# Kernel optimization log

Hardware: AMD Instinct MI355X
Metric: run time of the kernel (lower is better)

Reference implementation:

```python
import jax, jax.numpy as jnp
import numpy as np

H, D = 12, 768
DH = D // H  # 64

def setup_inputs() -> dict:
    key = jax.random.key(0)
    ks = jax.random.split(key, 9)
    s = 0.02
    x  = jax.random.normal(ks[0], (8, 1024, D), dtype=jnp.float32)
    Wq = jax.random.normal(ks[1], (H, D, DH), dtype=jnp.float32) * s
    Wk = jax.random.normal(ks[2], (H, D, DH), dtype=jnp.float32) * s
    Wv = jax.random.normal(ks[3], (H, D, DH), dtype=jnp.float32) * s
    bq = jax.random.normal(ks[4], (H, DH), dtype=jnp.float32) * s
    bk = jax.random.normal(ks[5], (H, DH), dtype=jnp.float32) * s
    bv = jax.random.normal(ks[6], (H, DH), dtype=jnp.float32) * s
    Wo = jax.random.normal(ks[7], (D, D), dtype=jnp.float32) * s
    bo = jax.random.normal(ks[8], (D,), dtype=jnp.float32) * s
    return {"x": x, "Wq": Wq, "Wk": Wk, "Wv": Wv, "bq": bq, "bk": bk, "bv": bv, "Wo": Wo, "bo": bo}

def reference(x, Wq, Wk, Wv, bq, bk, bv, Wo, bo):
    # x: [B,S,D]; per-head projections batched over heads: [B,H,S,DH]
    q = jnp.einsum('bsd,hde->bhse', x, Wq) + bq[None, :, None, :]
    k = jnp.einsum('bsd,hde->bhse', x, Wk) + bk[None, :, None, :]
    v = jnp.einsum('bsd,hde->bhse', x, Wv) + bv[None, :, None, :]
    scores = jnp.einsum('bhse,bhte->bhst', q, k) / jnp.sqrt(jnp.float32(DH))
    probs = jax.nn.softmax(scores, axis=-1)  # dropout is identity (p=0 / eval)
    ctx = jnp.einsum('bhst,bhte->bhse', probs, v)  # [B,H,S,DH]
    B, _, S, _ = ctx.shape
    # concat heads along feature dim (head order matches torch cat order)
    ctx = jnp.transpose(ctx, (0, 2, 1, 3)).reshape(B, S, H * DH)
    out = jnp.einsum('bsd,de->bse', ctx, Wo) + bo
    return out
```

## Files before the change

### kernel.cpp

```cpp
#include <hip/hip_runtime.h>
#include <math.h>


constexpr int NB  = 8;
constexpr int SEQ = 1024;
constexpr int NH  = 12;
constexpr int DM  = 768;
constexpr int DHD = 64;
constexpr int MROWS = NB * SEQ;
constexpr int NQKV  = 3 * NH * DHD;

typedef __attribute__((ext_vector_type(8))) short short8;
typedef __attribute__((ext_vector_type(4))) float f32x4;

#define MFMA16(a,b,c) __builtin_amdgcn_mfma_f32_16x16x32_bf16((a),(b),(c),0,0,0)

#if __has_builtin(__builtin_amdgcn_exp2f)
#define EXP2(x) __builtin_amdgcn_exp2f(x)
#else
#define EXP2(x) exp2f(x)
#endif

__device__ __forceinline__ unsigned short f2bf(float f) {
    unsigned u = __float_as_uint(f);
    return (unsigned short)((u + 0x7fffu + ((u >> 16) & 1u)) >> 16);
}
__device__ __forceinline__ unsigned short f2bf_fast(float f) {
    return (unsigned short)((__float_as_uint(f) + 0x8000u) >> 16);
}

__device__ __forceinline__ void gl_lds16(const unsigned short* g, unsigned short* l) {
    __builtin_amdgcn_global_load_lds(
        (const __attribute__((address_space(1))) void*)g,
        (__attribute__((address_space(3))) void*)l, 16, 0, 0);
}

__device__ __forceinline__ void stageK(unsigned short* lds, const unsigned short* gbase,
                                       int i, int ln, int ldg) {
    int r    = i * 8 + (ln >> 3);
    int cpos = ln & 7;
    int cdat = (cpos - r) & 7;
    gl_lds16(gbase + (size_t)r * ldg + cdat * 8, lds + i * 512);
}
__device__ __forceinline__ short8 ldK(const unsigned short* buf, int row, int chunk) {
    int c = (chunk + row) & 7;
    return *(const short8*)&buf[row * 64 + c * 8];
}

__global__ __launch_bounds__(256) void prep_k(
    const float* __restrict__ x,
    const float* __restrict__ Wq, const float* __restrict__ Wk,
    const float* __restrict__ Wv, const float* __restrict__ Wo,
    unsigned short* __restrict__ xb, unsigned short* __restrict__ wt,
    unsigned short* __restrict__ wot) {
    __shared__ float tb[64][65];
    const int blk = blockIdx.x, tid = threadIdx.x;
    if (blk < 6144) {
        const int i = blk * 256 + tid;
        float4 v = ((const float4*)x)[i];
        ushort4 o;
        o.x = f2bf(v.x); o.y = f2bf(v.y); o.z = f2bf(v.z); o.w = f2bf(v.w);
        ((ushort4*)xb)[i] = o;
        return;
    }
    const int t = blk - 6144;
    const int job = t / 144, lb = t % 144;
    const float* W;
    unsigned short* dst;
    int C, r0, c0;
    if (job < 3) {
        const float* Ws = (job == 0) ? Wq : (job == 1 ? Wk : Wv);
        const int h = lb / 12, rb = lb % 12;
        W = Ws + (size_t)h * (DM * DHD);
        dst = wt + (size_t)(job * 12 + h) * (DM * DHD);
        C = DHD; r0 = rb * 64; c0 = 0;
    } else {
        W = Wo; dst = wot; C = DM;
        r0 = (lb / 12) * 64; c0 = (lb % 12) * 64;
    }
    const int rr = tid >> 2, cc = (tid & 3) * 16;
#pragma unroll
    for (int j = 0; j < 16; j += 4) {
        float4 v = *(const float4*)&W[(size_t)(r0 + rr) * C + c0 + cc + j];
        tb[rr][cc + j + 0] = v.x;
        tb[rr][cc + j + 1] = v.y;
        tb[rr][cc + j + 2] = v.z;
        tb[rr][cc + j + 3] = v.w;
    }
    __syncthreads();
#pragma unroll
    for (int j = 0; j < 16; ++j)
        dst[(size_t)(c0 + rr) * DM + r0 + cc + j] = f2bf(tb[cc + j][rr]);
}

__global__ __launch_bounds__(256, 3) void qkv_mfma_k(
    const unsigned short* __restrict__ xb, const unsigned short* __restrict__ wt,
    const float* __restrict__ bq, const float* __restrict__ bk, const float* __restrict__ bv,
    unsigned short* __restrict__ qb, unsigned short* __restrict__ kb,
    unsigned short* __restrict__ vT) {
    __shared__ unsigned short Ah[128 * 64], Bh[128 * 64];

    const int tid = threadIdx.x;
    const int wv = tid >> 6, ln = tid & 63, quad = ln >> 4, lnid = ln & 15;
    const int wvm = wv >> 1, wvn = wv & 1;
    const int row0 = blockIdx.x * 128, col0 = blockIdx.y * 128;
    const int sel = (col0 >= 2 * DM) ? 2 : (col0 >= DM ? 1 : 0);

    f32x4 acc[4][4];
#pragma unroll
    for (int i = 0; i < 4; ++i)
#pragma unroll
        for (int j = 0; j < 4; ++j) acc[i][j] = (f32x4){0.f, 0.f, 0.f, 0.f};

    const unsigned short* Ahg = xb + (size_t)row0 * DM;
    const unsigned short* Bhg = wt + (size_t)col0 * DM;
    constexpr int NIT = DM / 64;

    if (sel < 2) {
        for (int it = 0; it < NIT; ++it) {
            const int kc = it * 64;
            __syncthreads();
#pragma unroll
            for (int c = 0; c < 4; ++c) {
                stageK(Ah, Ahg + kc, wv * 4 + c, ln, DM);
                stageK(Bh, Bhg + kc, wv * 4 + c, ln, DM);
            }
            __syncthreads();
#pragma unroll
            for (int ks = 0; ks < 2; ++ks) {
                short8 a[4], b[4];
#pragma unroll
                for (int i = 0; i < 4; ++i)
                    a[i] = ldK(Ah, wvm * 64 + i * 16 + lnid, ks * 4 + quad);
#pragma unroll
                for (int j = 0; j < 4; ++j)
                    b[j] = ldK(Bh, wvn * 64 + j * 16 + lnid, ks * 4 + quad);
#pragma unroll
                for (int j = 0; j < 4; ++j)
#pragma unroll
                    for (int i = 0; i < 4; ++i)
                        acc[j][i] = MFMA16(b[j], a[i], acc[j][i]);
            }
        }
        const float scale = (sel == 0) ? 0.18033688011112042f : 1.0f;
        const float* bias = (sel == 0) ? bq : bk;
        unsigned short* oh = (sel == 0) ? qb : kb;
#pragma unroll
        for (int et = 0; et < 4; ++et) {
            const int e = col0 + wvn * 64 + et * 16 + quad * 4;
            const int he = e - sel * DM;
            const int hh2 = he >> 6, ee = he & 63;
            float4 bs = *(const float4*)&bias[he];
#pragma unroll
            for (int st = 0; st < 4; ++st) {
                const int srow = row0 + wvm * 64 + st * 16 + lnid;
                const int bb = srow >> 10, ss = srow & (SEQ - 1);
                ushort4 pk;
                pk.x = f2bf((acc[et][st][0] + bs.x) * scale);
                pk.y = f2bf((acc[et][st][1] + bs.y) * scale);
                pk.z = f2bf((acc[et][st][2] + bs.z) * scale);
                pk.w = f2bf((acc[et][st][3] + bs.w) * scale);
                *(ushort4*)&oh[((size_t)(bb * NH + hh2) * SEQ + ss) * DHD + ee] = pk;
            }
        }
    } else {
        for (int it = 0; it < NIT; ++it) {
            const int kc = it * 64;
            __syncthreads();
#pragma unroll
            for (int c = 0; c < 4; ++c) {
                stageK(Ah, Ahg + kc, wv * 4 + c, ln, DM);
                stageK(Bh, Bhg + kc, wv * 4 + c, ln, DM);
            }
            __syncthreads();
#pragma unroll
            for (int ks = 0; ks < 2; ++ks) {
                short8 a[4], b[4];
#pragma unroll
                for (int i = 0; i < 4; ++i)
                    a[i] = ldK(Ah, wvm * 64 + i * 16 + lnid, ks * 4 + quad);
#pragma unroll
                for (int j = 0; j < 4; ++j)
                    b[j] = ldK(Bh, wvn * 64 + j * 16 + lnid, ks * 4 + quad);
#pragma unroll
                for (int i = 0; i < 4; ++i)
#pragma unroll
                    for (int j = 0; j < 4; ++j)
                        acc[i][j] = MFMA16(a[i], b[j], acc[i][j]);
            }
        }
#pragma unroll
        for (int i = 0; i < 4; ++i) {
#pragma unroll
            for (int j = 0; j < 4; ++j) {
                const int col = col0 + wvn * 64 + j * 16 + lnid;
                const int he = col - 2 * DM;
                const int hh2 = he >> 6, ee = he & 63;
                const float bs = bv[he];
                const int srow = row0 + wvm * 64 + i * 16 + quad * 4;
                const int bb = srow >> 10, ss = srow & (SEQ - 1);
                ushort4 pk;
                pk.x = f2bf(acc[i][j][0] + bs);
                pk.y = f2bf(acc[i][j][1] + bs);
                pk.z = f2bf(acc[i][j][2] + bs);
                pk.w = f2bf(acc[i][j][3] + bs);
                *(ushort4*)&vT[((size_t)(bb * NH + hh2) * DHD + ee) * SEQ + ss] = pk;
            }
        }
    }
}

__global__ __launch_bounds__(512, 6) void attn_mfma_k(
    const unsigned short* __restrict__ qb, const unsigned short* __restrict__ kb,
    const unsigned short* __restrict__ vT, unsigned short* __restrict__ ctb) {
    __shared__ unsigned short ksh[2][64 * 64], vsm[2][64 * 64];
    __shared__ unsigned short ps[128 * 64];

    const int tid = threadIdx.x;
    const int wv = tid >> 6, ln = tid & 63, quad = ln >> 4, lnid = ln & 15;
    const int bhid = blockIdx.x % 96, qt = blockIdx.x / 96;
    const int b = bhid / NH, h = bhid % NH;
    const int q0 = qt * 128;
    const unsigned short* qhb = qb + (size_t)bhid * (SEQ * DHD);
    const unsigned short* khb = kb + (size_t)bhid * (SEQ * DHD);
    const unsigned short* vTb = vT + (size_t)bhid * (DHD * SEQ);

    const int prow = wv * 16 + lnid;

    short8 qf[2];
#pragma unroll
    for (int ks_ = 0; ks_ < 2; ++ks_)
        qf[ks_] = *(const short8*)(qhb + (size_t)(q0 + prow) * DHD + ks_ * 32 + quad * 8);

    f32x4 ctx[4];
#pragma unroll
    for (int j = 0; j < 4; ++j) ctx[j] = (f32x4){0.f, 0.f, 0.f, 0.f};
    float lsum = 0.f;

    stageK(ksh[0], khb, wv, ln, DHD);
    stageK(vsm[0], vTb, wv, ln, SEQ);

    for (int kt = 0; kt < SEQ / 64; ++kt) {
        const int cur = kt & 1;
        __syncthreads();
        if (kt + 1 < SEQ / 64) {
            stageK(ksh[cur ^ 1], khb + (kt + 1) * 64 * DHD, wv, ln, DHD);
            stageK(vsm[cur ^ 1], vTb + (kt + 1) * 64, wv, ln, SEQ);
        }

        f32x4 sc[4];
#pragma unroll
        for (int j = 0; j < 4; ++j) sc[j] = (f32x4){0.f, 0.f, 0.f, 0.f};
#pragma unroll
        for (int ks_ = 0; ks_ < 2; ++ks_) {
#pragma unroll
            for (int nt = 0; nt < 4; ++nt) {
                short8 kf = ldK(ksh[cur], nt * 16 + lnid, ks_ * 4 + quad);
                sc[nt] = MFMA16(kf, qf[ks_], sc[nt]);
            }
        }

#pragma unroll
        for (int nt = 0; nt < 4; ++nt) {
            float p0 = EXP2(sc[nt][0]);
            float p1 = EXP2(sc[nt][1]);
            float p2 = EXP2(sc[nt][2]);
            float p3 = EXP2(sc[nt][3]);
            lsum += (p0 + p1) + (p2 + p3);
            ushort4 pw;
            pw.x = f2bf_fast(p0);
            pw.y = f2bf_fast(p1);
            pw.z = f2bf_fast(p2);
            pw.w = f2bf_fast(p3);
            const int cpos = (2 * nt + (quad >> 1) + prow) & 7;
            *(ushort4*)&ps[prow * 64 + cpos * 8 + (quad & 1) * 4] = pw;
        }

#pragma unroll
        for (int kvs = 0; kvs < 2; ++kvs) {
            short8 pf = ldK(ps, prow, kvs * 4 + quad);
#pragma unroll
            for (int dt = 0; dt < 4; ++dt) {
                short8 vf = ldK(vsm[cur], dt * 16 + lnid, kvs * 4 + quad);
                ctx[dt] = MFMA16(vf, pf, ctx[dt]);
            }
        }
    }

    float s = lsum;
    s += __shfl_xor(s, 16, 64);
    s += __shfl_xor(s, 32, 64);
    const float inv = 1.0f / s;
    const int srow = b * SEQ + q0 + prow;
#pragma unroll
    for (int dt = 0; dt < 4; ++dt) {
        ushort4 pk;
        pk.x = f2bf(ctx[dt][0] * inv);
        pk.y = f2bf(ctx[dt][1] * inv);
        pk.z = f2bf(ctx[dt][2] * inv);
        pk.w = f2bf(ctx[dt][3] * inv);
        *(ushort4*)&ctb[(size_t)srow * DM + h * DHD + dt * 16 + quad * 4] = pk;
    }
}

__global__ __launch_bounds__(256, 3) void out_mfma_k(
    const unsigned short* __restrict__ ctb, const unsigned short* __restrict__ wot,
    const float* __restrict__ bo, float* __restrict__ out) {
    __shared__ unsigned short Ah[128 * 64], Bh[64 * 64];

    const int tid = threadIdx.x;
    const int wv = tid >> 6, ln = tid & 63, quad = ln >> 4, lnid = ln & 15;
    const int wvm = wv >> 1, wvn = wv & 1;
    const int row0 = blockIdx.x * 128, col0 = blockIdx.y * 64;

    f32x4 acc[2][4];
#pragma unroll
    for (int j = 0; j < 2; ++j)
#pragma unroll
        for (int i = 0; i < 4; ++i) acc[j][i] = (f32x4){0.f, 0.f, 0.f, 0.f};

    const unsigned short* Ahg = ctb + (size_t)row0 * DM;
    const unsigned short* Bhg = wot + (size_t)col0 * DM;

    constexpr int NIT = DM / 64;
    for (int it = 0; it < NIT; ++it) {
        const int kc = it * 64;
        __syncthreads();
#pragma unroll
        for (int c = 0; c < 4; ++c) stageK(Ah, Ahg + kc, wv * 4 + c, ln, DM);
#pragma unroll
        for (int c = 0; c < 2; ++c) stageK(Bh, Bhg + kc, wv * 2 + c, ln, DM);
        __syncthreads();
#pragma unroll
        for (int ks = 0; ks < 2; ++ks) {
            short8 a[4], b[2];
#pragma unroll
            for (int i = 0; i < 4; ++i)
                a[i] = ldK(Ah, wvm * 64 + i * 16 + lnid, ks * 4 + quad);
#pragma unroll
            for (int j = 0; j < 2; ++j)
                b[j] = ldK(Bh, wvn * 32 + j * 16 + lnid, ks * 4 + quad);
#pragma unroll
            for (int j = 0; j < 2; ++j)
#pragma unroll
                for (int i = 0; i < 4; ++i)
                    acc[j][i] = MFMA16(b[j], a[i], acc[j][i]);
        }
    }

#pragma unroll
    for (int jt = 0; jt < 2; ++jt) {
        const int colb = col0 + wvn * 32 + jt * 16 + quad * 4;
        float4 bs = *(const float4*)&bo[colb];
#pragma unroll
        for (int it = 0; it < 4; ++it) {
            const int srow = row0 + wvm * 64 + it * 16 + lnid;
            float4 o;
            o.x = acc[jt][it][0] + bs.x;
            o.y = acc[jt][it][1] + bs.y;
            o.z = acc[jt][it][2] + bs.z;
            o.w = acc[jt][it][3] + bs.w;
            *(float4*)&out[(size_t)srow * DM + colb] = o;
        }
    }
}

extern "C" void kernel_launch(void* const* d_in, const int* in_sizes, int n_in,
                              void* d_out, int out_size, void* d_ws, size_t ws_size,
                              hipStream_t stream) {
    const float* x  = (const float*)d_in[0];
    const float* Wq = (const float*)d_in[1];
    const float* Wk = (const float*)d_in[2];
    const float* Wv = (const float*)d_in[3];
    const float* bq = (const float*)d_in[4];
    const float* bk = (const float*)d_in[5];
    const float* bv = (const float*)d_in[6];
    const float* Wo = (const float*)d_in[7];
    const float* bo = (const float*)d_in[8];
    float* out = (float*)d_out;

    char* w = (char*)d_ws;
    const size_t elsX = (size_t)MROWS * DM;
    const size_t elsQ = (size_t)NB * NH * SEQ * DHD;
    unsigned short* xb  = (unsigned short*)w;
    unsigned short* ctb = xb;
    size_t off = elsX * 2;
    unsigned short* wt  = (unsigned short*)(w + off); off += (size_t)NQKV * DM * 2;
    unsigned short* wot = (unsigned short*)(w + off); off += (size_t)DM * DM * 2;
    unsigned short* qbp = (unsigned short*)(w + off); off += elsQ * 2;
    unsigned short* kbp = (unsigned short*)(w + off); off += elsQ * 2;
    unsigned short* vTp = (unsigned short*)(w + off); off += elsQ * 2;

    prep_k<<<dim3(6144 + 576), 256, 0, stream>>>(x, Wq, Wk, Wv, Wo, xb, wt, wot);
    qkv_mfma_k<<<dim3(MROWS / 128, NQKV / 128), 256, 0, stream>>>(
        xb, wt, bq, bk, bv, qbp, kbp, vTp);
    attn_mfma_k<<<dim3(768), 512, 0, stream>>>(qbp, kbp, vTp, ctb);
    out_mfma_k<<<dim3(MROWS / 128, DM / 64), 256, 0, stream>>>(ctb, wot, bo, out);
}
```

Before: 192.1 us.

## Give each attention wave two 16-row query groups to reuse K/V fragments

The attention kernel moves from 8 waves of 16 query rows to 4 waves of 32 query rows. Each wave keeps two sets of Q fragments and accumulators, so every K and V fragment loaded from LDS feeds two MFMAs. This cuts LDS reads per MFMA and the number of waves in each block, and each wave now does twice the staging work. The cost is higher register pressure and less wave-level parallelism for hiding latency, with launch bounds changed to (256, 3).

```diff
diff --git a/kernel.cpp b/kernel.cpp
--- a/kernel.cpp
+++ b/kernel.cpp
@@ -210,7 +210,7 @@
     }
 }
 
-__global__ __launch_bounds__(512, 6) void attn_mfma_k(
+__global__ __launch_bounds__(256, 3) void attn_mfma_k(
     const unsigned short* __restrict__ qb, const unsigned short* __restrict__ kb,
     const unsigned short* __restrict__ vT, unsigned short* __restrict__ ctb) {
     __shared__ unsigned short ksh[2][64 * 64], vsm[2][64 * 64];
@@ -225,81 +225,103 @@
     const unsigned short* khb = kb + (size_t)bhid * (SEQ * DHD);
     const unsigned short* vTb = vT + (size_t)bhid * (DHD * SEQ);
 
-    const int prow = wv * 16 + lnid;
-
-    short8 qf[2];
-#pragma unroll
-    for (int ks_ = 0; ks_ < 2; ++ks_)
-        qf[ks_] = *(const short8*)(qhb + (size_t)(q0 + prow) * DHD + ks_ * 32 + quad * 8);
-
-    f32x4 ctx[4];
-#pragma unroll
-    for (int j = 0; j < 4; ++j) ctx[j] = (f32x4){0.f, 0.f, 0.f, 0.f};
-    float lsum = 0.f;
-
-    stageK(ksh[0], khb, wv, ln, DHD);
-    stageK(vsm[0], vTb, wv, ln, SEQ);
+    const int prow0 = wv * 32 + lnid;
+
+    short8 qf[2][2];
+#pragma unroll
+    for (int rg = 0; rg < 2; ++rg)
+#pragma unroll
+        for (int ks_ = 0; ks_ < 2; ++ks_)
+            qf[rg][ks_] = *(const short8*)(qhb +
+                (size_t)(q0 + prow0 + rg * 16) * DHD + ks_ * 32 + quad * 8);
+
+    f32x4 ctx[2][4];
+#pragma unroll
+    for (int rg = 0; rg < 2; ++rg)
+#pragma unroll
+        for (int j = 0; j < 4; ++j) ctx[rg][j] = (f32x4){0.f, 0.f, 0.f, 0.f};
+    float lsum0 = 0.f, lsum1 = 0.f;
+
+    stageK(ksh[0], khb, wv * 2 + 0, ln, DHD);
+    stageK(ksh[0], khb, wv * 2 + 1, ln, DHD);
+    stageK(vsm[0], vTb, wv * 2 + 0, ln, SEQ);
+    stageK(vsm[0], vTb, wv * 2 + 1, ln, SEQ);
 
     for (int kt = 0; kt < SEQ / 64; ++kt) {
         const int cur = kt & 1;
         __syncthreads();
         if (kt + 1 < SEQ / 64) {
-            stageK(ksh[cur ^ 1], khb + (kt + 1) * 64 * DHD, wv, ln, DHD);
-            stageK(vsm[cur ^ 1], vTb + (kt + 1) * 64, wv, ln, SEQ);
-        }
-
-        f32x4 sc[4];
-#pragma unroll
-        for (int j = 0; j < 4; ++j) sc[j] = (f32x4){0.f, 0.f, 0.f, 0.f};
+            stageK(ksh[cur ^ 1], khb + (kt + 1) * 64 * DHD, wv * 2 + 0, ln, DHD);
+            stageK(ksh[cur ^ 1], khb + (kt + 1) * 64 * DHD, wv * 2 + 1, ln, DHD);
+            stageK(vsm[cur ^ 1], vTb + (kt + 1) * 64, wv * 2 + 0, ln, SEQ);
+            stageK(vsm[cur ^ 1], vTb + (kt + 1) * 64, wv * 2 + 1, ln, SEQ);
+        }
+
+        f32x4 sc[2][4];
+#pragma unroll
+        for (int rg = 0; rg < 2; ++rg)
+#pragma unroll
+            for (int j = 0; j < 4; ++j) sc[rg][j] = (f32x4){0.f, 0.f, 0.f, 0.f};
 #pragma unroll
         for (int ks_ = 0; ks_ < 2; ++ks_) {
 #pragma unroll
             for (int nt = 0; nt < 4; ++nt) {
                 short8 kf = ldK(ksh[cur], nt * 16 + lnid, ks_ * 4 + quad);
-                sc[nt] = MFMA16(kf, qf[ks_], sc[nt]);
-            }
-        }
-
-#pragma unroll
-        for (int nt = 0; nt < 4; ++nt) {
-            float p0 = EXP2(sc[nt][0]);
-            float p1 = EXP2(sc[nt][1]);
-            float p2 = EXP2(sc[nt][2]);
-            float p3 = EXP2(sc[nt][3]);
-            lsum += (p0 + p1) + (p2 + p3);
-            ushort4 pw;
-            pw.x = f2bf_fast(p0);
-            pw.y = f2bf_fast(p1);
-            pw.z = f2bf_fast(p2);
-            pw.w = f2bf_fast(p3);
-            const int cpos = (2 * nt + (quad >> 1) + prow) & 7;
-            *(ushort4*)&ps[prow * 64 + cpos * 8 + (quad & 1) * 4] = pw;
+                sc[0][nt] = MFMA16(kf, qf[0][ks_], sc[0][nt]);
+                sc[1][nt] = MFMA16(kf, qf[1][ks_], sc[1][nt]);
+            }
+        }
+
+#pragma unroll
+        for (int rg = 0; rg < 2; ++rg) {
+            const int prow = prow0 + rg * 16;
+#pragma unroll
+            for (int nt = 0; nt < 4; ++nt) {
+                float p0 = EXP2(sc[rg][nt][0]);
+                float p1 = EXP2(sc[rg][nt][1]);
+                float p2 = EXP2(sc[rg][nt][2]);
+                float p3 = EXP2(sc[rg][nt][3]);
+                if (rg == 0) lsum0 += (p0 + p1) + (p2 + p3);
+                else         lsum1 += (p0 + p1) + (p2 + p3);
+                ushort4 pw;
+                pw.x = f2bf_fast(p0);
+                pw.y = f2bf_fast(p1);
+                pw.z = f2bf_fast(p2);
+                pw.w = f2bf_fast(p3);
+                const int cpos = (2 * nt + (quad >> 1) + prow) & 7;
+                *(ushort4*)&ps[prow * 64 + cpos * 8 + (quad & 1) * 4] = pw;
+            }
         }
 
 #pragma unroll
         for (int kvs = 0; kvs < 2; ++kvs) {
-            short8 pf = ldK(ps, prow, kvs * 4 + quad);
+            short8 pf0 = ldK(ps, prow0,      kvs * 4 + quad);
+            short8 pf1 = ldK(ps, prow0 + 16, kvs * 4 + quad);
 #pragma unroll
             for (int dt = 0; dt < 4; ++dt) {
                 short8 vf = ldK(vsm[cur], dt * 16 + lnid, kvs * 4 + quad);
-                ctx[dt] = MFMA16(vf, pf, ctx[dt]);
-            }
-        }
-    }
-
-    float s = lsum;
-    s += __shfl_xor(s, 16, 64);
-    s += __shfl_xor(s, 32, 64);
-    const float inv = 1.0f / s;
-    const int srow = b * SEQ + q0 + prow;
-#pragma unroll
-    for (int dt = 0; dt < 4; ++dt) {
-        ushort4 pk;
-        pk.x = f2bf(ctx[dt][0] * inv);
-        pk.y = f2bf(ctx[dt][1] * inv);
-        pk.z = f2bf(ctx[dt][2] * inv);
-        pk.w = f2bf(ctx[dt][3] * inv);
-        *(ushort4*)&ctb[(size_t)srow * DM + h * DHD + dt * 16 + quad * 4] = pk;
+                ctx[0][dt] = MFMA16(vf, pf0, ctx[0][dt]);
+                ctx[1][dt] = MFMA16(vf, pf1, ctx[1][dt]);
+            }
+        }
+    }
+
+#pragma unroll
+    for (int rg = 0; rg < 2; ++rg) {
+        float s = (rg == 0) ? lsum0 : lsum1;
+        s += __shfl_xor(s, 16, 64);
+        s += __shfl_xor(s, 32, 64);
+        const float inv = 1.0f / s;
+        const int srow = b * SEQ + q0 + prow0 + rg * 16;
+#pragma unroll
+        for (int dt = 0; dt < 4; ++dt) {
+            ushort4 pk;
+            pk.x = f2bf(ctx[rg][dt][0] * inv);
+            pk.y = f2bf(ctx[rg][dt][1] * inv);
+            pk.z = f2bf(ctx[rg][dt][2] * inv);
+            pk.w = f2bf(ctx[rg][dt][3] * inv);
+            *(ushort4*)&ctb[(size_t)srow * DM + h * DHD + dt * 16 + quad * 4] = pk;
+        }
     }
 }
 
@@ -394,6 +416,6 @@
     prep_k<<<dim3(6144 + 576), 256, 0, stream>>>(x, Wq, Wk, Wv, Wo, xb, wt, wot);
     qkv_mfma_k<<<dim3(MROWS / 128, NQKV / 128), 256, 0, stream>>>(
         xb, wt, bq, bk, bv, qbp, kbp, vTp);
-    attn_mfma_k<<<dim3(768), 512, 0, stream>>>(qbp, kbp, vTp, ctb);
+    attn_mfma_k<<<dim3(768), 256, 0, stream>>>(qbp, kbp, vTp, ctb);
     out_mfma_k<<<dim3(MROWS / 128, DM / 64), 256, 0, stream>>>(ctb, wot, bo, out);
 }
```

After: 191.7 us. About the same (-0.2%).

## Switch attention to 32x32x16 MFMA with 256-query tiles per block

Applied to the files above, without the earlier changes.

The attention kernel now uses 32x32x16 bf16 MFMA instructions instead of 16x16x32, and each wave owns 32 query rows, so a block covers 256 queries and the grid is halved. Each K/V tile staged into LDS is therefore reused across twice as many queries, cutting global and LDS traffic per unit of work. In exchange the P buffer in LDS doubles, register pressure rises (16-wide accumulators), occupancy is lowered to 4 blocks, and only 384 blocks are launched, which may underfill the GPU.

```diff
diff --git a/kernel.cpp b/kernel.cpp
--- a/kernel.cpp
+++ b/kernel.cpp
@@ -12,8 +12,10 @@
 
 typedef __attribute__((ext_vector_type(8))) short short8;
 typedef __attribute__((ext_vector_type(4))) float f32x4;
+typedef __attribute__((ext_vector_type(16))) float f32x16;
 
 #define MFMA16(a,b,c) __builtin_amdgcn_mfma_f32_16x16x32_bf16((a),(b),(c),0,0,0)
+#define MFMA32(a,b,c) __builtin_amdgcn_mfma_f32_32x32x16_bf16((a),(b),(c),0,0,0)
 
 #if __has_builtin(__builtin_amdgcn_exp2f)
 #define EXP2(x) __builtin_amdgcn_exp2f(x)
@@ -210,31 +212,33 @@
     }
 }
 
-__global__ __launch_bounds__(512, 6) void attn_mfma_k(
+__global__ __launch_bounds__(512, 4) void attn_mfma_k(
     const unsigned short* __restrict__ qb, const unsigned short* __restrict__ kb,
     const unsigned short* __restrict__ vT, unsigned short* __restrict__ ctb) {
     __shared__ unsigned short ksh[2][64 * 64], vsm[2][64 * 64];
-    __shared__ unsigned short ps[128 * 64];
+    __shared__ unsigned short ps[256 * 64];
 
     const int tid = threadIdx.x;
-    const int wv = tid >> 6, ln = tid & 63, quad = ln >> 4, lnid = ln & 15;
+    const int wv = tid >> 6, ln = tid & 63, lo5 = ln & 31, hi = ln >> 5;
     const int bhid = blockIdx.x % 96, qt = blockIdx.x / 96;
     const int b = bhid / NH, h = bhid % NH;
-    const int q0 = qt * 128;
+    const int q0 = qt * 256;
     const unsigned short* qhb = qb + (size_t)bhid * (SEQ * DHD);
     const unsigned short* khb = kb + (size_t)bhid * (SEQ * DHD);
     const unsigned short* vTb = vT + (size_t)bhid * (DHD * SEQ);
 
-    const int prow = wv * 16 + lnid;
-
-    short8 qf[2];
-#pragma unroll
-    for (int ks_ = 0; ks_ < 2; ++ks_)
-        qf[ks_] = *(const short8*)(qhb + (size_t)(q0 + prow) * DHD + ks_ * 32 + quad * 8);
-
-    f32x4 ctx[4];
-#pragma unroll
-    for (int j = 0; j < 4; ++j) ctx[j] = (f32x4){0.f, 0.f, 0.f, 0.f};
+    const int wq = wv * 32 + lo5;
+
+    short8 qf[4];
+#pragma unroll
+    for (int ds = 0; ds < 4; ++ds)
+        qf[ds] = *(const short8*)(qhb + (size_t)(q0 + wq) * DHD + ds * 16 + hi * 8);
+
+    f32x16 ctx[2];
+#pragma unroll
+    for (int dt = 0; dt < 2; ++dt)
+#pragma unroll
+        for (int r = 0; r < 16; ++r) ctx[dt][r] = 0.f;
     float lsum = 0.f;
 
     stageK(ksh[0], khb, wv, ln, DHD);
@@ -248,58 +252,63 @@
             stageK(vsm[cur ^ 1], vTb + (kt + 1) * 64, wv, ln, SEQ);
         }
 
-        f32x4 sc[4];
-#pragma unroll
-        for (int j = 0; j < 4; ++j) sc[j] = (f32x4){0.f, 0.f, 0.f, 0.f};
-#pragma unroll
-        for (int ks_ = 0; ks_ < 2; ++ks_) {
-#pragma unroll
-            for (int nt = 0; nt < 4; ++nt) {
-                short8 kf = ldK(ksh[cur], nt * 16 + lnid, ks_ * 4 + quad);
-                sc[nt] = MFMA16(kf, qf[ks_], sc[nt]);
-            }
-        }
-
-#pragma unroll
-        for (int nt = 0; nt < 4; ++nt) {
-            float p0 = EXP2(sc[nt][0]);
-            float p1 = EXP2(sc[nt][1]);
-            float p2 = EXP2(sc[nt][2]);
-            float p3 = EXP2(sc[nt][3]);
-            lsum += (p0 + p1) + (p2 + p3);
-            ushort4 pw;
-            pw.x = f2bf_fast(p0);
-            pw.y = f2bf_fast(p1);
-            pw.z = f2bf_fast(p2);
-            pw.w = f2bf_fast(p3);
-            const int cpos = (2 * nt + (quad >> 1) + prow) & 7;
-            *(ushort4*)&ps[prow * 64 + cpos * 8 + (quad & 1) * 4] = pw;
-        }
-
-#pragma unroll
-        for (int kvs = 0; kvs < 2; ++kvs) {
-            short8 pf = ldK(ps, prow, kvs * 4 + quad);
-#pragma unroll
-            for (int dt = 0; dt < 4; ++dt) {
-                short8 vf = ldK(vsm[cur], dt * 16 + lnid, kvs * 4 + quad);
-                ctx[dt] = MFMA16(vf, pf, ctx[dt]);
-            }
-        }
-    }
-
-    float s = lsum;
-    s += __shfl_xor(s, 16, 64);
-    s += __shfl_xor(s, 32, 64);
+        f32x16 sc[2];
+#pragma unroll
+        for (int kk = 0; kk < 2; ++kk) {
+#pragma unroll
+            for (int r = 0; r < 16; ++r) sc[kk][r] = 0.f;
+#pragma unroll
+            for (int ds = 0; ds < 4; ++ds) {
+                short8 kf = ldK(ksh[cur], kk * 32 + lo5, ds * 2 + hi);
+                sc[kk] = MFMA32(kf, qf[ds], sc[kk]);
+            }
+        }
+
+#pragma unroll
+        for (int kk = 0; kk < 2; ++kk) {
+#pragma unroll
+            for (int m = 0; m < 4; ++m) {
+                float p0 = EXP2(sc[kk][4 * m + 0]);
+                float p1 = EXP2(sc[kk][4 * m + 1]);
+                float p2 = EXP2(sc[kk][4 * m + 2]);
+                float p3 = EXP2(sc[kk][4 * m + 3]);
+                lsum += (p0 + p1) + (p2 + p3);
+                ushort4 pw;
+                pw.x = f2bf_fast(p0);
+                pw.y = f2bf_fast(p1);
+                pw.z = f2bf_fast(p2);
+                pw.w = f2bf_fast(p3);
+                const int c = kk * 4 + m;
+                const int pc = (c + wq) & 7;
+                *(ushort4*)&ps[wq * 64 + pc * 8 + hi * 4] = pw;
+            }
+        }
+
+#pragma unroll
+        for (int step = 0; step < 4; ++step) {
+            short8 pf = ldK(ps, wq, step * 2 + hi);
+#pragma unroll
+            for (int dt = 0; dt < 2; ++dt) {
+                short8 vf = ldK(vsm[cur], dt * 32 + lo5, step * 2 + hi);
+                ctx[dt] = MFMA32(vf, pf, ctx[dt]);
+            }
+        }
+    }
+
+    float s = lsum + __shfl_xor(lsum, 32, 64);
     const float inv = 1.0f / s;
-    const int srow = b * SEQ + q0 + prow;
-#pragma unroll
-    for (int dt = 0; dt < 4; ++dt) {
-        ushort4 pk;
-        pk.x = f2bf(ctx[dt][0] * inv);
-        pk.y = f2bf(ctx[dt][1] * inv);
-        pk.z = f2bf(ctx[dt][2] * inv);
-        pk.w = f2bf(ctx[dt][3] * inv);
-        *(ushort4*)&ctb[(size_t)srow * DM + h * DHD + dt * 16 + quad * 4] = pk;
+    const int srow = b * SEQ + q0 + wq;
+#pragma unroll
+    for (int dt = 0; dt < 2; ++dt) {
+#pragma unroll
+        for (int m = 0; m < 4; ++m) {
+            ushort4 pk;
+            pk.x = f2bf(ctx[dt][4 * m + 0] * inv);
+            pk.y = f2bf(ctx[dt][4 * m + 1] * inv);
+            pk.z = f2bf(ctx[dt][4 * m + 2] * inv);
+            pk.w = f2bf(ctx[dt][4 * m + 3] * inv);
+            *(ushort4*)&ctb[(size_t)srow * DM + h * DHD + dt * 32 + m * 8 + hi * 4] = pk;
+        }
     }
 }
 
@@ -394,6 +403,6 @@
     prep_k<<<dim3(6144 + 576), 256, 0, stream>>>(x, Wq, Wk, Wv, Wo, xb, wt, wot);
     qkv_mfma_k<<<dim3(MROWS / 128, NQKV / 128), 256, 0, stream>>>(
         xb, wt, bq, bk, bv, qbp, kbp, vTp);
-    attn_mfma_k<<<dim3(768), 512, 0, stream>>>(qbp, kbp, vTp, ctb);
+    attn_mfma_k<<<dim3(384), 512, 0, stream>>>(qbp, kbp, vTp, ctb);
     out_mfma_k<<<dim3(MROWS / 128, DM / 64), 256, 0, stream>>>(ctb, wot, bo, out);
 }
```

After: 194.3 us. About the same (+1.1%).

## Double-buffer LDS tiles in QKV GEMM to overlap staging with MFMA

Applied to the files above, without the earlier changes.

The QKV projection kernel now keeps two LDS buffers for the A and B tiles. It stages the next K-chunk into the alternate buffer while the MFMAs consume the current one, which drops one barrier per iteration. The aim is to hide global-load and LDS-store latency behind compute. In exchange, LDS use per block doubles and launch bounds fall from 3 to 2 blocks per CU, so occupancy is lower.

```diff
diff --git a/kernel.cpp b/kernel.cpp
--- a/kernel.cpp
+++ b/kernel.cpp
@@ -93,12 +93,12 @@
         dst[(size_t)(c0 + rr) * DM + r0 + cc + j] = f2bf(tb[cc + j][rr]);
 }
 
-__global__ __launch_bounds__(256, 3) void qkv_mfma_k(
+__global__ __launch_bounds__(256, 2) void qkv_mfma_k(
     const unsigned short* __restrict__ xb, const unsigned short* __restrict__ wt,
     const float* __restrict__ bq, const float* __restrict__ bk, const float* __restrict__ bv,
     unsigned short* __restrict__ qb, unsigned short* __restrict__ kb,
     unsigned short* __restrict__ vT) {
-    __shared__ unsigned short Ah[128 * 64], Bh[128 * 64];
+    __shared__ unsigned short Ah[2][128 * 64], Bh[2][128 * 64];
 
     const int tid = threadIdx.x;
     const int wv = tid >> 6, ln = tid & 63, quad = ln >> 4, lnid = ln & 15;
@@ -116,25 +116,33 @@
     const unsigned short* Bhg = wt + (size_t)col0 * DM;
     constexpr int NIT = DM / 64;
 
+#pragma unroll
+    for (int c = 0; c < 4; ++c) {
+        stageK(Ah[0], Ahg, wv * 4 + c, ln, DM);
+        stageK(Bh[0], Bhg, wv * 4 + c, ln, DM);
+    }
+
     if (sel < 2) {
         for (int it = 0; it < NIT; ++it) {
-            const int kc = it * 64;
+            const int cur = it & 1;
             __syncthreads();
-#pragma unroll
-            for (int c = 0; c < 4; ++c) {
-                stageK(Ah, Ahg + kc, wv * 4 + c, ln, DM);
-                stageK(Bh, Bhg + kc, wv * 4 + c, ln, DM);
-            }
-            __syncthreads();
+            if (it + 1 < NIT) {
+                const int kc = (it + 1) * 64;
+#pragma unroll
+                for (int c = 0; c < 4; ++c) {
+                    stageK(Ah[cur ^ 1], Ahg + kc, wv * 4 + c, ln, DM);
+                    stageK(Bh[cur ^ 1], Bhg + kc, wv * 4 + c, ln, DM);
+                }
+            }
 #pragma unroll
             for (int ks = 0; ks < 2; ++ks) {
                 short8 a[4], b[4];
 #pragma unroll
                 for (int i = 0; i < 4; ++i)
-                    a[i] = ldK(Ah, wvm * 64 + i * 16 + lnid, ks * 4 + quad);
+                    a[i] = ldK(Ah[cur], wvm * 64 + i * 16 + lnid, ks * 4 + quad);
 #pragma unroll
                 for (int j = 0; j < 4; ++j)
-                    b[j] = ldK(Bh, wvn * 64 + j * 16 + lnid, ks * 4 + quad);
+                    b[j] = ldK(Bh[cur], wvn * 64 + j * 16 + lnid, ks * 4 + quad);
 #pragma unroll
                 for (int j = 0; j < 4; ++j)
 #pragma unroll
@@ -165,23 +173,25 @@
         }
     } else {
         for (int it = 0; it < NIT; ++it) {
-            const int kc = it * 64;
+            const int cur = it & 1;
             __syncthreads();
-#pragma unroll
-            for (int c = 0; c < 4; ++c) {
-                stageK(Ah, Ahg + kc, wv * 4 + c, ln, DM);
-                stageK(Bh, Bhg + kc, wv * 4 + c, ln, DM);
-            }
-            __syncthreads();
+            if (it + 1 < NIT) {
+                const int kc = (it + 1) * 64;
+#pragma unroll
+                for (int c = 0; c < 4; ++c) {
+                    stageK(Ah[cur ^ 1], Ahg + kc, wv * 4 + c, ln, DM);
+                    stageK(Bh[cur ^ 1], Bhg + kc, wv * 4 + c, ln, DM);
+                }
+            }
 #pragma unroll
             for (int ks = 0; ks < 2; ++ks) {
                 short8 a[4], b[4];
 #pragma unroll
                 for (int i = 0; i < 4; ++i)
-                    a[i] = ldK(Ah, wvm * 64 + i * 16 + lnid, ks * 4 + quad);
+                    a[i] = ldK(Ah[cur], wvm * 64 + i * 16 + lnid, ks * 4 + quad);
 #pragma unroll
                 for (int j = 0; j < 4; ++j)
-                    b[j] = ldK(Bh, wvn * 64 + j * 16 + lnid, ks * 4 + quad);
+                    b[j] = ldK(Bh[cur], wvn * 64 + j * 16 + lnid, ks * 4 + quad);
 #pragma unroll
                 for (int i = 0; i < 4; ++i)
 #pragma unroll
```

Result: slower. 198.5 us (+3.3%).
